# Optimization experiments

Hardware: AMD Instinct MI355X
Metric: run time of the kernel (lower is better)

The kernel has to match this reference:

```python
import jax, jax.numpy as jnp
import numpy as np
import math

B, L, S, H, E, D = 8, 2048, 2048, 8, 64, 64


def setup_inputs() -> dict:
    key = jax.random.key(0)
    kq, kk, kv = jax.random.split(key, 3)
    return {
        "queries": jax.random.normal(kq, (B, L, H, E), dtype=jnp.float32),
        "keys": jax.random.normal(kk, (B, S, H, E), dtype=jnp.float32),
        "values": jax.random.normal(kv, (B, S, H, D), dtype=jnp.float32),
        "attn_mask": jnp.zeros((B, L, S), dtype=bool),
    }


def reference(queries, keys, values, attn_mask):
    b, l, h, e = queries.shape
    s, d = values.shape[1], values.shape[3]
    scale = 1.0 / math.sqrt(e)  # note: 1/sqrt(E), not 1/sqrt(H*E), faithful to source
    q = queries.reshape(b, l, h * e)            # [B, L, HE]
    k = keys.reshape(b, s, h * e)               # [B, S, HE]
    scores = jnp.einsum("ble,bse->bls", q, k)   # full [B, L, S] score matrix
    scores = jnp.where(attn_mask, -jnp.inf, scores)
    A = jax.nn.softmax(scale * scores, axis=-1)  # dropout is identity at inference
    v = values.reshape(b, s, h * d)             # [B, S, HD]
    out = jnp.einsum("bls,bsd->bld", A, v).reshape(b, l, h, d)
    return out
```

## Files before the change

### kernel.cpp

```cpp
#include <hip/hip_runtime.h>
#include <hip/hip_bf16.h>
#include <stdint.h>

typedef __attribute__((ext_vector_type(8))) short  short8;
typedef __attribute__((ext_vector_type(4))) short  short4v;
typedef __attribute__((ext_vector_type(8))) __bf16 bf16x8;
typedef __attribute__((ext_vector_type(4))) float  f32x4;

#define DEVI static __device__ __forceinline__

constexpr int B_  = 8;
constexpr int L_  = 2048;
constexpr int S_  = 2048;
constexpr int DK  = 512;
constexpr int KVB = 32;
constexpr int QB  = 64;
constexpr int NT  = S_ / KVB;
constexpr int TILE_B = KVB * DK * 2;
constexpr float SCL2 = 0.125f * 1.4426950408889634f;

constexpr size_t KT_OFF = 0;
constexpr size_t VT_OFF = (size_t)B_ * NT * TILE_B;
constexpr size_t AM_OFF = VT_OFF * 2;
constexpr size_t WS_NEED = AM_OFF + (size_t)B_ * L_ * 8;

DEVI short f2bf(float f) {
  __hip_bfloat16 h = __float2bfloat16(f);
  return __builtin_bit_cast(short, h);
}

DEVI void gld16(const void* g, void* l) {
  __builtin_amdgcn_global_load_lds(
      (const __attribute__((address_space(1))) unsigned int*)(uintptr_t)g,
      (__attribute__((address_space(3))) unsigned int*)(uint32_t)(uintptr_t)l,
      16, 0, 0);
}


__global__ __launch_bounds__(256)
void prep_k(const float* __restrict__ K, char* __restrict__ Kt) {
  int gid  = blockIdx.x * 256 + threadIdx.x;
  int o    = (gid & 2047) * 16;
  int tile = gid >> 11;
  int row  = o >> 10;
  int colb = (o & 1023) ^ ((row & 7) << 4);
  const float* src = K + ((size_t)tile * KVB + row) * DK + (colb >> 1);
  float4 a = ((const float4*)src)[0];
  float4 c = ((const float4*)src)[1];
  short8 f;
  f[0] = f2bf(a.x); f[1] = f2bf(a.y); f[2] = f2bf(a.z); f[3] = f2bf(a.w);
  f[4] = f2bf(c.x); f[5] = f2bf(c.y); f[6] = f2bf(c.z); f[7] = f2bf(c.w);
  *(short8*)(Kt + (size_t)tile * TILE_B + o) = f;
}

__global__ __launch_bounds__(256)
void prep_v(const float* __restrict__ V, char* __restrict__ Vt) {
  __shared__ short lv[KVB * DK];
  int tile = blockIdx.x;
  int tid  = threadIdx.x;
  const float* src = V + (size_t)tile * KVB * DK;
  #pragma unroll
  for (int i = 0; i < 16; ++i) {
    int fidx = i * 1024 + tid * 4;
    float4 v = *(const float4*)(src + fidx);
    short4v pk = { f2bf(v.x), f2bf(v.y), f2bf(v.z), f2bf(v.w) };
    *(short4v*)((char*)lv + (size_t)fidx * 2) = pk;
  }
  __syncthreads();
  char* dst = Vt + (size_t)tile * TILE_B;
  #pragma unroll
  for (int j = 0; j < 8; ++j) {
    int o     = tid * 16 + j * 4096;
    int pr    = o >> 7;
    int inner = (o & 127) ^ ((pr & 7) << 4);
    int d     = pr * 2 + (inner >> 6);
    int kv0   = (inner & 63) >> 1;
    short8 f;
    #pragma unroll
    for (int k = 0; k < 8; ++k) f[k] = lv[(kv0 + k) * DK + d];
    *(short8*)(dst + o) = f;
  }
}

__global__ __launch_bounds__(256)
void prep_mask(const unsigned char* __restrict__ M,
               unsigned long long* __restrict__ anyM) {
  int row = blockIdx.x * 4 + (threadIdx.x >> 6);
  int l   = threadIdx.x & 63;
  const unsigned int* p = (const unsigned int*)(M + (size_t)row * S_) + l * 8;
  unsigned int acc = 0;
  #pragma unroll
  for (int k = 0; k < 8; ++k) acc |= p[k];
  unsigned long long bal = __ballot(acc != 0);
  if (l == 0) anyM[row] = bal;
}


__global__ __launch_bounds__(256, 1)
void fattn2(const float* __restrict__ Qg, const char* __restrict__ Kt,
            const char* __restrict__ Vt, const unsigned long long* __restrict__ anyM,
            const unsigned char* __restrict__ Mg, float* __restrict__ Og) {
  __shared__ __attribute__((aligned(16))) char kv_lds[2][2 * TILE_B];
  __shared__ __attribute__((aligned(16))) short pbuf[4][16 * KVB];

  const int tid = threadIdx.x;
  const int w   = tid >> 6;
  const int l   = tid & 63;
  const int l15 = l & 15;
  const int l4  = l >> 4;

  const int bidx = blockIdx.x;
  const int swz  = ((bidx & 7) << 5) + (bidx >> 3);
  const int b    = swz >> 5;
  const int qt   = swz & 31;
  const int qloc = qt * QB + w * 16;

  bf16x8 qf[16];
  {
    const float* qp = Qg + ((size_t)(b * L_ + qloc + l15)) * DK + l4 * 8;
    #pragma unroll
    for (int c = 0; c < 16; ++c) {
      float4 a  = *(const float4*)(qp + c * 32);
      float4 bq = *(const float4*)(qp + c * 32 + 4);
      short8 f;
      f[0] = f2bf(a.x);  f[1] = f2bf(a.y);  f[2] = f2bf(a.z);  f[3] = f2bf(a.w);
      f[4] = f2bf(bq.x); f[5] = f2bf(bq.y); f[6] = f2bf(bq.z); f[7] = f2bf(bq.w);
      qf[c] = __builtin_bit_cast(bf16x8, f);
    }
  }
  const unsigned long long mbits = anyM[(size_t)b * L_ + qloc + l15];

  f32x4 acc[32];
  #pragma unroll
  for (int i = 0; i < 32; ++i) acc[i] = f32x4{0.f, 0.f, 0.f, 0.f};
  float mrow[4] = {-__builtin_inff(), -__builtin_inff(), -__builtin_inff(), -__builtin_inff()};
  float lrow[4] = {0.f, 0.f, 0.f, 0.f};

  const char* Ktb = Kt + (size_t)b * NT * TILE_B;
  const char* Vtb = Vt + (size_t)b * NT * TILE_B;
  const unsigned char* Mb = Mg + (size_t)b * L_ * S_;

  const int bKu  = (l15 << 10) + (l4 << 4);
  const int swzK = (l15 & 7) << 4;
  const int bV = (((l15 >> 1) << 7) + ((l15 & 1) << 6) + (l4 << 4)) ^ (((l15 >> 1) & 7) << 4);
  const int bP = l15 * 64 + l4 * 16;

  auto stage = [&](int t, char* buf) {
    const char* ks = Ktb + (size_t)t * TILE_B + w * 1024 + l * 16;
    const char* vs = Vtb + (size_t)t * TILE_B + w * 1024 + l * 16;
    char* kd = buf + w * 1024;
    char* vd = buf + TILE_B + w * 1024;
    #pragma unroll
    for (int r = 0; r < 8; ++r) gld16(ks + r * 4096, kd + r * 4096);
    #pragma unroll
    for (int r = 0; r < 8; ++r) gld16(vs + r * 4096, vd + r * 4096);
  };

  stage(0, kv_lds[0]);
  stage(1, kv_lds[1]);

  for (int t = 0; t < NT; ++t) {
    if (t < NT - 1) asm volatile("s_waitcnt vmcnt(16)" ::: "memory");
    else            asm volatile("s_waitcnt vmcnt(0)"  ::: "memory");
    __builtin_amdgcn_s_barrier();
    asm volatile("" ::: "memory");

    const char* kb = kv_lds[t & 1];
    const char* vb = kv_lds[t & 1] + TILE_B;

    f32x4 s0a = f32x4{0.f, 0.f, 0.f, 0.f};
    f32x4 s0b = f32x4{0.f, 0.f, 0.f, 0.f};
    f32x4 s1a = f32x4{0.f, 0.f, 0.f, 0.f};
    f32x4 s1b = f32x4{0.f, 0.f, 0.f, 0.f};
    #pragma unroll
    for (int c = 0; c < 16; c += 2) {
      int a0 = (bKu + c * 64) ^ swzK;
      int a1 = (bKu + (c + 1) * 64) ^ swzK;
      bf16x8 k0f = *(const bf16x8*)(kb + a0);
      bf16x8 k0g = *(const bf16x8*)(kb + a1);
      bf16x8 k1f = *(const bf16x8*)(kb + a0 + 16384);
      bf16x8 k1g = *(const bf16x8*)(kb + a1 + 16384);
      s0a = __builtin_amdgcn_mfma_f32_16x16x32_bf16(qf[c],     k0f, s0a, 0, 0, 0);
      s1a = __builtin_amdgcn_mfma_f32_16x16x32_bf16(qf[c],     k1f, s1a, 0, 0, 0);
      s0b = __builtin_amdgcn_mfma_f32_16x16x32_bf16(qf[c + 1], k0g, s0b, 0, 0, 0);
      s1b = __builtin_amdgcn_mfma_f32_16x16x32_bf16(qf[c + 1], k1g, s1b, 0, 0, 0);
    }
    float sv0[4], sv1[4];
    #pragma unroll
    for (int r = 0; r < 4; ++r) { sv0[r] = s0a[r] + s0b[r]; sv1[r] = s1a[r] + s1b[r]; }

    if (__any((mbits >> t) & 1ull)) {
      #pragma unroll
      for (int r = 0; r < 4; ++r) {
        const unsigned char* mp = Mb + (size_t)(qloc + l4 * 4 + r) * S_ + (t * KVB + l15);
        if (mp[0])  sv0[r] = -__builtin_inff();
        if (mp[16]) sv1[r] = -__builtin_inff();
      }
    }

    bool need = false;
    float alpha[4];
    #pragma unroll
    for (int r = 0; r < 4; ++r) {
      float tmax = fmaxf(sv0[r], sv1[r]);
      #pragma unroll
      for (int mk = 1; mk < 16; mk <<= 1) tmax = fmaxf(tmax, __shfl_xor(tmax, mk));
      alpha[r] = 1.0f;
      if (tmax > mrow[r]) {
        if ((tmax - mrow[r]) * SCL2 > 8.0f) {
          alpha[r] = exp2f((mrow[r] - tmax) * SCL2);
          mrow[r] = tmax;
          need = true;
        }
      }
    }
    if (__any(need)) {
      #pragma unroll
      for (int dt = 0; dt < 32; ++dt) {
        acc[dt][0] *= alpha[0];
        acc[dt][1] *= alpha[1];
        acc[dt][2] *= alpha[2];
        acc[dt][3] *= alpha[3];
      }
      lrow[0] *= alpha[0]; lrow[1] *= alpha[1];
      lrow[2] *= alpha[2]; lrow[3] *= alpha[3];
    }

    short* pw = pbuf[w];
    #pragma unroll
    for (int r = 0; r < 4; ++r) {
      float p0 = exp2f((sv0[r] - mrow[r]) * SCL2);
      float p1 = exp2f((sv1[r] - mrow[r]) * SCL2);
      lrow[r] += p0 + p1;
      int pr = (l4 * 4 + r) * 32;
      pw[pr + l15]      = f2bf(p0);
      pw[pr + 16 + l15] = f2bf(p1);
    }
    bf16x8 pf = *(const bf16x8*)((const char*)pw + bP);

    #pragma unroll
    for (int dt = 0; dt < 32; ++dt) {
      bf16x8 vf = *(const bf16x8*)(vb + bV + dt * 1024);
      acc[dt] = __builtin_amdgcn_mfma_f32_16x16x32_bf16(pf, vf, acc[dt], 0, 0, 0);
    }

    asm volatile("" ::: "memory");
    __builtin_amdgcn_s_barrier();
    if (t + 2 < NT) stage(t + 2, kv_lds[t & 1]);
  }

  #pragma unroll
  for (int r = 0; r < 4; ++r) {
    float s = lrow[r];
    #pragma unroll
    for (int mk = 1; mk < 16; mk <<= 1) s += __shfl_xor(s, mk);
    lrow[r] = 1.0f / s;
  }
  float* op = Og + ((size_t)(b * L_ + qloc + l4 * 4)) * DK + l15;
  #pragma unroll
  for (int r = 0; r < 4; ++r) {
    #pragma unroll
    for (int dt = 0; dt < 32; ++dt) {
      op[(size_t)r * DK + dt * 16] = acc[dt][r] * lrow[r];
    }
  }
}


__global__ __launch_bounds__(256, 2)
void fattn_kernel(const float* __restrict__ Qg, const float* __restrict__ Kg,
                  const float* __restrict__ Vg, const unsigned char* __restrict__ Mg,
                  float* __restrict__ Og) {
  __shared__ __attribute__((aligned(16))) short kbuf[KVB * DK];
  __shared__ __attribute__((aligned(16))) short vbuf[KVB * DK];
  __shared__ __attribute__((aligned(16))) short pbuf[4][16 * KVB];

  const int tid = threadIdx.x;
  const int w   = tid >> 6;
  const int l   = tid & 63;
  const int l15 = l & 15;
  const int l4  = l >> 4;

  const int b    = blockIdx.y;
  const int qloc = blockIdx.x * QB + w * 16;

  bf16x8 qf[16];
  {
    const float* qp = Qg + ((size_t)(b * L_ + qloc + l15)) * DK + l4 * 8;
    #pragma unroll
    for (int c = 0; c < 16; ++c) {
      float4 a  = *(const float4*)(qp + c * 32);
      float4 bq = *(const float4*)(qp + c * 32 + 4);
      short8 f;
      f[0] = f2bf(a.x);  f[1] = f2bf(a.y);  f[2] = f2bf(a.z);  f[3] = f2bf(a.w);
      f[4] = f2bf(bq.x); f[5] = f2bf(bq.y); f[6] = f2bf(bq.z); f[7] = f2bf(bq.w);
      qf[c] = __builtin_bit_cast(bf16x8, f);
    }
  }

  f32x4 acc[32];
  #pragma unroll
  for (int i = 0; i < 32; ++i) acc[i] = f32x4{0.f, 0.f, 0.f, 0.f};
  float mrow[4] = {-__builtin_inff(), -__builtin_inff(), -__builtin_inff(), -__builtin_inff()};
  float lrow[4] = {0.f, 0.f, 0.f, 0.f};

  const float* Kb = Kg + (size_t)b * S_ * DK;
  const float* Vb = Vg + (size_t)b * S_ * DK;
  const unsigned char* Mb = Mg + (size_t)b * L_ * S_;

  const int bKu  = (l15 << 10) + (l4 << 4);
  const int swzK = (l15 & 7) << 4;
  const int bV = (((l15 >> 1) << 7) + ((l15 & 1) << 6) + (l4 << 4)) ^ (((l15 >> 1) & 7) << 4);
  const int bP = l15 * 64 + l4 * 16;

  for (int t = 0; t < S_ / KVB; ++t) {
    const int k0 = t * KVB;
    {
      const float* src = Kb + (size_t)k0 * DK;
      #pragma unroll
      for (int it = 0; it < 16; ++it) {
        int fidx = it * 1024 + tid * 4;
        float4 v = *(const float4*)(src + fidx);
        int row = fidx >> 9;
        int col = fidx & 511;
        int byt = ((row << 10) + (col << 1)) ^ ((row & 7) << 4);
        short4v pk = { f2bf(v.x), f2bf(v.y), f2bf(v.z), f2bf(v.w) };
        *(short4v*)((char*)kbuf + byt) = pk;
      }
    }
    {
      const float* src = Vb + (size_t)k0 * DK;
      #pragma unroll
      for (int h = 0; h < 4; ++h) {
        int task = h * 256 + tid;
        int dblk = task & 127;
        int kvb  = task >> 7;
        const float* sp = src + (size_t)(kvb * 4) * DK + dblk * 4;
        float4 r0 = *(const float4*)(sp);
        float4 r1 = *(const float4*)(sp + DK);
        float4 r2 = *(const float4*)(sp + 2 * DK);
        float4 r3 = *(const float4*)(sp + 3 * DK);
        #pragma unroll
        for (int i = 0; i < 4; ++i) {
          int d = dblk * 4 + i;
          int byt = (((d >> 1) << 7) + ((d & 1) << 6) + ((kvb * 4) << 1))
                    ^ (((d >> 1) & 7) << 4);
          float e0 = (i == 0) ? r0.x : (i == 1) ? r0.y : (i == 2) ? r0.z : r0.w;
          float e1 = (i == 0) ? r1.x : (i == 1) ? r1.y : (i == 2) ? r1.z : r1.w;
          float e2 = (i == 0) ? r2.x : (i == 1) ? r2.y : (i == 2) ? r2.z : r2.w;
          float e3 = (i == 0) ? r3.x : (i == 1) ? r3.y : (i == 2) ? r3.z : r3.w;
          short4v pk = { f2bf(e0), f2bf(e1), f2bf(e2), f2bf(e3) };
          *(short4v*)((char*)vbuf + byt) = pk;
        }
      }
    }
    __syncthreads();

    f32x4 s0a = f32x4{0.f, 0.f, 0.f, 0.f};
    f32x4 s0b = f32x4{0.f, 0.f, 0.f, 0.f};
    f32x4 s1a = f32x4{0.f, 0.f, 0.f, 0.f};
    f32x4 s1b = f32x4{0.f, 0.f, 0.f, 0.f};
    #pragma unroll
    for (int c = 0; c < 16; c += 2) {
      int a0 = (bKu + c * 64) ^ swzK;
      int a1 = (bKu + (c + 1) * 64) ^ swzK;
      bf16x8 k0f = *(const bf16x8*)((const char*)kbuf + a0);
      bf16x8 k0g = *(const bf16x8*)((const char*)kbuf + a1);
      bf16x8 k1f = *(const bf16x8*)((const char*)kbuf + a0 + 16384);
      bf16x8 k1g = *(const bf16x8*)((const char*)kbuf + a1 + 16384);
      s0a = __builtin_amdgcn_mfma_f32_16x16x32_bf16(qf[c],     k0f, s0a, 0, 0, 0);
      s1a = __builtin_amdgcn_mfma_f32_16x16x32_bf16(qf[c],     k1f, s1a, 0, 0, 0);
      s0b = __builtin_amdgcn_mfma_f32_16x16x32_bf16(qf[c + 1], k0g, s0b, 0, 0, 0);
      s1b = __builtin_amdgcn_mfma_f32_16x16x32_bf16(qf[c + 1], k1g, s1b, 0, 0, 0);
    }
    f32x4 s0, s1;
    #pragma unroll
    for (int r = 0; r < 4; ++r) { s0[r] = s0a[r] + s0b[r]; s1[r] = s1a[r] + s1b[r]; }

    float sv0[4], sv1[4];
    #pragma unroll
    for (int r = 0; r < 4; ++r) {
      const unsigned char* mp = Mb + (size_t)(qloc + l4 * 4 + r) * S_ + (k0 + l15);
      float x0 = s0[r], x1 = s1[r];
      if (mp[0])  x0 = -__builtin_inff();
      if (mp[16]) x1 = -__builtin_inff();
      sv0[r] = x0; sv1[r] = x1;
    }

    bool need = false;
    float alpha[4];
    #pragma unroll
    for (int r = 0; r < 4; ++r) {
      float tmax = fmaxf(sv0[r], sv1[r]);
      #pragma unroll
      for (int mk = 1; mk < 16; mk <<= 1) tmax = fmaxf(tmax, __shfl_xor(tmax, mk));
      alpha[r] = 1.0f;
      if (tmax > mrow[r]) {
        if ((tmax - mrow[r]) * SCL2 > 8.0f) {
          alpha[r] = exp2f((mrow[r] - tmax) * SCL2);
          mrow[r] = tmax;
          need = true;
        }
      }
    }
    if (__any(need)) {
      #pragma unroll
      for (int dt = 0; dt < 32; ++dt) {
        acc[dt][0] *= alpha[0];
        acc[dt][1] *= alpha[1];
        acc[dt][2] *= alpha[2];
        acc[dt][3] *= alpha[3];
      }
      lrow[0] *= alpha[0]; lrow[1] *= alpha[1];
      lrow[2] *= alpha[2]; lrow[3] *= alpha[3];
    }

    short* pw = pbuf[w];
    #pragma unroll
    for (int r = 0; r < 4; ++r) {
      float p0 = exp2f((sv0[r] - mrow[r]) * SCL2);
      float p1 = exp2f((sv1[r] - mrow[r]) * SCL2);
      lrow[r] += p0 + p1;
      int pr = (l4 * 4 + r) * 32;
      pw[pr + l15]      = f2bf(p0);
      pw[pr + 16 + l15] = f2bf(p1);
    }
    bf16x8 pf = *(const bf16x8*)((const char*)pw + bP);

    #pragma unroll
    for (int dt = 0; dt < 32; ++dt) {
      bf16x8 vf = *(const bf16x8*)((const char*)vbuf + (bV + dt * 1024));
      acc[dt] = __builtin_amdgcn_mfma_f32_16x16x32_bf16(pf, vf, acc[dt], 0, 0, 0);
    }
    __syncthreads();
  }

  #pragma unroll
  for (int r = 0; r < 4; ++r) {
    float s = lrow[r];
    #pragma unroll
    for (int mk = 1; mk < 16; mk <<= 1) s += __shfl_xor(s, mk);
    lrow[r] = 1.0f / s;
  }
  float* op = Og + ((size_t)(b * L_ + qloc + l4 * 4)) * DK + l15;
  #pragma unroll
  for (int r = 0; r < 4; ++r) {
    #pragma unroll
    for (int dt = 0; dt < 32; ++dt) {
      op[(size_t)r * DK + dt * 16] = acc[dt][r] * lrow[r];
    }
  }
}


extern "C" void kernel_launch(void* const* d_in, const int* in_sizes, int n_in,
                              void* d_out, int out_size, void* d_ws, size_t ws_size,
                              hipStream_t stream) {
  const float* Q = (const float*)d_in[0];
  const float* K = (const float*)d_in[1];
  const float* V = (const float*)d_in[2];
  const unsigned char* M = (const unsigned char*)d_in[3];
  float* O = (float*)d_out;

  if (ws_size >= WS_NEED) {
    char* ws = (char*)d_ws;
    prep_k   <<<4096, 256, 0, stream>>>(K, ws + KT_OFF);
    prep_v   <<<B_ * NT, 256, 0, stream>>>(V, ws + VT_OFF);
    prep_mask<<<B_ * L_ / 4, 256, 0, stream>>>(M, (unsigned long long*)(ws + AM_OFF));
    fattn2   <<<256, 256, 0, stream>>>(Q, ws + KT_OFF, ws + VT_OFF,
                                       (const unsigned long long*)(ws + AM_OFF), M, O);
  } else {
    dim3 grid(L_ / QB, B_);
    fattn_kernel<<<grid, 256, 0, stream>>>(Q, K, V, M, O);
  }
}
```

Measured before the change: 224.7 us.

## Split KV sequence across two wave groups per block with LDS merge

```diff
diff --git a/kernel.cpp b/kernel.cpp
--- a/kernel.cpp
+++ b/kernel.cpp
@@ -16,6 +16,7 @@
 constexpr int KVB = 32;
 constexpr int QB  = 64;
 constexpr int NT  = S_ / KVB;
+constexpr int NT2 = NT / 2;
 constexpr int TILE_B = KVB * DK * 2;
 constexpr float SCL2 = 0.125f * 1.4426950408889634f;
 
@@ -23,6 +24,14 @@
 constexpr size_t VT_OFF = (size_t)B_ * NT * TILE_B;
 constexpr size_t AM_OFF = VT_OFF * 2;
 constexpr size_t WS_NEED = AM_OFF + (size_t)B_ * L_ * 8;
+
+constexpr int LDS_K0  = 0;
+constexpr int LDS_K1  = 32768;
+constexpr int LDS_V0  = 65536;
+constexpr int LDS_V1  = 98304;
+constexpr int LDS_PB  = 131072;
+constexpr int LDS_MEX = 140288;
+constexpr int LDS_TOT = 141312;
 
 DEVI short f2bf(float f) {
   __hip_bfloat16 h = __float2bfloat16(f);
@@ -96,15 +105,16 @@
 }
 
 
-__global__ __launch_bounds__(256, 1)
-void fattn2(const float* __restrict__ Qg, const char* __restrict__ Kt,
+__global__ __launch_bounds__(512, 2)
+void fattn3(const float* __restrict__ Qg, const char* __restrict__ Kt,
             const char* __restrict__ Vt, const unsigned long long* __restrict__ anyM,
             const unsigned char* __restrict__ Mg, float* __restrict__ Og) {
-  __shared__ __attribute__((aligned(16))) char kv_lds[2][2 * TILE_B];
-  __shared__ __attribute__((aligned(16))) short pbuf[4][16 * KVB];
+  __shared__ __attribute__((aligned(16))) char LDS[LDS_TOT];
 
   const int tid = threadIdx.x;
   const int w   = tid >> 6;
+  const int wl  = w & 3;
+  const int g   = w >> 2;
   const int l   = tid & 63;
   const int l15 = l & 15;
   const int l4  = l >> 4;
@@ -113,7 +123,7 @@
   const int swz  = ((bidx & 7) << 5) + (bidx >> 3);
   const int b    = swz >> 5;
   const int qt   = swz & 31;
-  const int qloc = qt * QB + w * 16;
+  const int qloc = qt * QB + wl * 16;
 
   bf16x8 qf[16];
   {
@@ -140,33 +150,37 @@
   const char* Vtb = Vt + (size_t)b * NT * TILE_B;
   const unsigned char* Mb = Mg + (size_t)b * L_ * S_;
 
+  const char* kb = LDS + (g ? LDS_K1 : LDS_K0);
+  const char* vb = LDS + (g ? LDS_V1 : LDS_V0);
+  short* pw = (short*)(LDS + LDS_PB) + w * (16 * 36);
+
   const int bKu  = (l15 << 10) + (l4 << 4);
   const int swzK = (l15 & 7) << 4;
   const int bV = (((l15 >> 1) << 7) + ((l15 & 1) << 6) + (l4 << 4)) ^ (((l15 >> 1) & 7) << 4);
-  const int bP = l15 * 64 + l4 * 16;
-
-  auto stage = [&](int t, char* buf) {
-    const char* ks = Ktb + (size_t)t * TILE_B + w * 1024 + l * 16;
-    const char* vs = Vtb + (size_t)t * TILE_B + w * 1024 + l * 16;
-    char* kd = buf + w * 1024;
-    char* vd = buf + TILE_B + w * 1024;
-    #pragma unroll
-    for (int r = 0; r < 8; ++r) gld16(ks + r * 4096, kd + r * 4096);
-    #pragma unroll
-    for (int r = 0; r < 8; ++r) gld16(vs + r * 4096, vd + r * 4096);
+  const int bP = l15 * 72 + l4 * 16;
+
+  auto stageK = [&](int t) {
+    const char* ks = Ktb + (size_t)t * TILE_B + wl * 8192 + l * 16;
+    char* kd = (char*)kb + wl * 8192;
+    #pragma unroll
+    for (int r = 0; r < 8; ++r) gld16(ks + r * 1024, kd + r * 1024);
   };
-
-  stage(0, kv_lds[0]);
-  stage(1, kv_lds[1]);
-
-  for (int t = 0; t < NT; ++t) {
-    if (t < NT - 1) asm volatile("s_waitcnt vmcnt(16)" ::: "memory");
-    else            asm volatile("s_waitcnt vmcnt(0)"  ::: "memory");
+  auto stageV = [&](int t) {
+    const char* vs = Vtb + (size_t)t * TILE_B + wl * 8192 + l * 16;
+    char* vd = (char*)vb + wl * 8192;
+    #pragma unroll
+    for (int r = 0; r < 8; ++r) gld16(vs + r * 1024, vd + r * 1024);
+  };
+
+  stageK(g);
+  stageV(g);
+
+  for (int i = 0; i < NT2; ++i) {
+    const int t = 2 * i + g;
+
+    asm volatile("s_waitcnt vmcnt(8)" ::: "memory");
     __builtin_amdgcn_s_barrier();
     asm volatile("" ::: "memory");
-
-    const char* kb = kv_lds[t & 1];
-    const char* vb = kv_lds[t & 1] + TILE_B;
 
     f32x4 s0a = f32x4{0.f, 0.f, 0.f, 0.f};
     f32x4 s0b = f32x4{0.f, 0.f, 0.f, 0.f};
@@ -189,6 +203,10 @@
     #pragma unroll
     for (int r = 0; r < 4; ++r) { sv0[r] = s0a[r] + s0b[r]; sv1[r] = s1a[r] + s1b[r]; }
 
+    asm volatile("" ::: "memory");
+    __builtin_amdgcn_s_barrier();
+    if (i + 1 < NT2) stageK(t + 2);
+
     if (__any((mbits >> t) & 1ull)) {
       #pragma unroll
       for (int r = 0; r < 4; ++r) {
@@ -226,17 +244,21 @@
       lrow[2] *= alpha[2]; lrow[3] *= alpha[3];
     }
 
-    short* pw = pbuf[w];
     #pragma unroll
     for (int r = 0; r < 4; ++r) {
       float p0 = exp2f((sv0[r] - mrow[r]) * SCL2);
       float p1 = exp2f((sv1[r] - mrow[r]) * SCL2);
       lrow[r] += p0 + p1;
-      int pr = (l4 * 4 + r) * 32;
+      int pr = (l4 * 4 + r) * 36;
       pw[pr + l15]      = f2bf(p0);
       pw[pr + 16 + l15] = f2bf(p1);
     }
     bf16x8 pf = *(const bf16x8*)((const char*)pw + bP);
+
+    if (i + 1 < NT2) asm volatile("s_waitcnt vmcnt(8)" ::: "memory");
+    else             asm volatile("s_waitcnt vmcnt(0)" ::: "memory");
+    __builtin_amdgcn_s_barrier();
+    asm volatile("" ::: "memory");
 
     #pragma unroll
     for (int dt = 0; dt < 32; ++dt) {
@@ -246,7 +268,7 @@
 
     asm volatile("" ::: "memory");
     __builtin_amdgcn_s_barrier();
-    if (t + 2 < NT) stage(t + 2, kv_lds[t & 1]);
+    if (i + 1 < NT2) stageV(t + 2);
   }
 
   #pragma unroll
@@ -254,14 +276,56 @@
     float s = lrow[r];
     #pragma unroll
     for (int mk = 1; mk < 16; mk <<= 1) s += __shfl_xor(s, mk);
-    lrow[r] = 1.0f / s;
-  }
+    lrow[r] = s;
+  }
+
+  float* mex = (float*)(LDS + LDS_MEX);
+  if (l15 == 0) {
+    #pragma unroll
+    for (int r = 0; r < 4; ++r) {
+      mex[(w * 16 + l4 * 4 + r) * 2 + 0] = mrow[r];
+      mex[(w * 16 + l4 * 4 + r) * 2 + 1] = lrow[r];
+    }
+  }
+  asm volatile("" ::: "memory");
+  __builtin_amdgcn_s_barrier();
+  asm volatile("" ::: "memory");
+
+  const int pwav = w ^ 4;
+  float asf[4], linv[4];
+  #pragma unroll
+  for (int r = 0; r < 4; ++r) {
+    float mo = mex[(pwav * 16 + l4 * 4 + r) * 2 + 0];
+    float lo = mex[(pwav * 16 + l4 * 4 + r) * 2 + 1];
+    float mst = fmaxf(mrow[r], mo);
+    float a_s = exp2f((mrow[r] - mst) * SCL2);
+    float a_o = exp2f((mo - mst) * SCL2);
+    asf[r]  = a_s;
+    linv[r] = 1.0f / (a_s * lrow[r] + a_o * lo);
+  }
+
+  float* mg = (float*)LDS + (size_t)wl * (16 * 521);
+  const int dbase = g ? 16 : 0;
+  #pragma unroll
+  for (int r = 0; r < 4; ++r) {
+    #pragma unroll
+    for (int dt = 0; dt < 16; ++dt) {
+      mg[(l4 * 4 + r) * 521 + (dbase + dt) * 16 + l15] = asf[r] * acc[dbase + dt][r];
+    }
+  }
+  asm volatile("" ::: "memory");
+  __builtin_amdgcn_s_barrier();
+  asm volatile("" ::: "memory");
+
+  const int sbase = g ? 0 : 16;
   float* op = Og + ((size_t)(b * L_ + qloc + l4 * 4)) * DK + l15;
   #pragma unroll
   for (int r = 0; r < 4; ++r) {
     #pragma unroll
-    for (int dt = 0; dt < 32; ++dt) {
-      op[(size_t)r * DK + dt * 16] = acc[dt][r] * lrow[r];
+    for (int dt = 0; dt < 16; ++dt) {
+      int dd = sbase + dt;
+      float v = (asf[r] * acc[dd][r] + mg[(l4 * 4 + r) * 521 + dd * 16 + l15]) * linv[r];
+      op[(size_t)r * DK + dd * 16] = v;
     }
   }
 }
@@ -415,17 +479,17 @@
       lrow[2] *= alpha[2]; lrow[3] *= alpha[3];
     }
 
-    short* pw = pbuf[w];
+    short* pws = pbuf[w];
     #pragma unroll
     for (int r = 0; r < 4; ++r) {
       float p0 = exp2f((sv0[r] - mrow[r]) * SCL2);
       float p1 = exp2f((sv1[r] - mrow[r]) * SCL2);
       lrow[r] += p0 + p1;
       int pr = (l4 * 4 + r) * 32;
-      pw[pr + l15]      = f2bf(p0);
-      pw[pr + 16 + l15] = f2bf(p1);
-    }
-    bf16x8 pf = *(const bf16x8*)((const char*)pw + bP);
+      pws[pr + l15]      = f2bf(p0);
+      pws[pr + 16 + l15] = f2bf(p1);
+    }
+    bf16x8 pf = *(const bf16x8*)((const char*)pws + bP);
 
     #pragma unroll
     for (int dt = 0; dt < 32; ++dt) {
@@ -467,7 +531,7 @@
     prep_k   <<<4096, 256, 0, stream>>>(K, ws + KT_OFF);
     prep_v   <<<B_ * NT, 256, 0, stream>>>(V, ws + VT_OFF);
     prep_mask<<<B_ * L_ / 4, 256, 0, stream>>>(M, (unsigned long long*)(ws + AM_OFF));
-    fattn2   <<<256, 256, 0, stream>>>(Q, ws + KT_OFF, ws + VT_OFF,
+    fattn3   <<<256, 512, 0, stream>>>(Q, ws + KT_OFF, ws + VT_OFF,
                                        (const unsigned long long*)(ws + AM_OFF), M, O);
   } else {
     dim3 grid(L_ / QB, B_);
```

Result: slower. 331.0 us (+47.3%).

## Split attention work across wave pairs, halving QK depth and PV width per wave

Applied to the files above, without the earlier changes.

```diff
diff --git a/kernel.cpp b/kernel.cpp
--- a/kernel.cpp
+++ b/kernel.cpp
@@ -23,6 +23,12 @@
 constexpr size_t VT_OFF = (size_t)B_ * NT * TILE_B;
 constexpr size_t AM_OFF = VT_OFF * 2;
 constexpr size_t WS_NEED = AM_OFF + (size_t)B_ * L_ * 8;
+
+constexpr int LDS_BUF0 = 0;
+constexpr int LDS_BUF1 = 65536;
+constexpr int LDS_SX   = 131072;
+constexpr int LDS_PB   = 147456;
+constexpr int LDS_TOT  = 152064;
 
 DEVI short f2bf(float f) {
   __hip_bfloat16 h = __float2bfloat16(f);
@@ -97,53 +103,67 @@
 
 
 __global__ __launch_bounds__(256, 1)
-void fattn2(const float* __restrict__ Qg, const char* __restrict__ Kt,
+void fattn4(const float* __restrict__ Qg, const char* __restrict__ Kt,
             const char* __restrict__ Vt, const unsigned long long* __restrict__ anyM,
             const unsigned char* __restrict__ Mg, float* __restrict__ Og) {
-  __shared__ __attribute__((aligned(16))) char kv_lds[2][2 * TILE_B];
-  __shared__ __attribute__((aligned(16))) short pbuf[4][16 * KVB];
-
-  const int tid = threadIdx.x;
-  const int w   = tid >> 6;
-  const int l   = tid & 63;
-  const int l15 = l & 15;
-  const int l4  = l >> 4;
+  __shared__ __attribute__((aligned(16))) char LDS[LDS_TOT];
+
+  const int tid  = threadIdx.x;
+  const int w    = tid >> 6;
+  const int pair = w >> 1;
+  const int half = w & 1;
+  const int l    = tid & 63;
+  const int l15  = l & 15;
+  const int l4   = l >> 4;
 
   const int bidx = blockIdx.x;
   const int swz  = ((bidx & 7) << 5) + (bidx >> 3);
   const int b    = swz >> 5;
   const int qt   = swz & 31;
-  const int qloc = qt * QB + w * 16;
-
-  bf16x8 qf[16];
-  {
-    const float* qp = Qg + ((size_t)(b * L_ + qloc + l15)) * DK + l4 * 8;
-    #pragma unroll
-    for (int c = 0; c < 16; ++c) {
+  const int qrow = qt * QB + pair * 32;
+
+  bf16x8 qf[2][8];
+  #pragma unroll
+  for (int rg = 0; rg < 2; ++rg) {
+    const float* qp = Qg + ((size_t)(b * L_ + qrow + rg * 16 + l15)) * DK
+                      + half * 256 + l4 * 8;
+    #pragma unroll
+    for (int c = 0; c < 8; ++c) {
       float4 a  = *(const float4*)(qp + c * 32);
       float4 bq = *(const float4*)(qp + c * 32 + 4);
       short8 f;
       f[0] = f2bf(a.x);  f[1] = f2bf(a.y);  f[2] = f2bf(a.z);  f[3] = f2bf(a.w);
       f[4] = f2bf(bq.x); f[5] = f2bf(bq.y); f[6] = f2bf(bq.z); f[7] = f2bf(bq.w);
-      qf[c] = __builtin_bit_cast(bf16x8, f);
-    }
-  }
-  const unsigned long long mbits = anyM[(size_t)b * L_ + qloc + l15];
-
-  f32x4 acc[32];
-  #pragma unroll
-  for (int i = 0; i < 32; ++i) acc[i] = f32x4{0.f, 0.f, 0.f, 0.f};
-  float mrow[4] = {-__builtin_inff(), -__builtin_inff(), -__builtin_inff(), -__builtin_inff()};
-  float lrow[4] = {0.f, 0.f, 0.f, 0.f};
+      qf[rg][c] = __builtin_bit_cast(bf16x8, f);
+    }
+  }
+  const unsigned long long mb0 = anyM[(size_t)b * L_ + qrow + l15];
+  const unsigned long long mb1 = anyM[(size_t)b * L_ + qrow + 16 + l15];
+  const unsigned long long mbAny = mb0 | mb1;
+
+  f32x4 acc[2][16];
+  #pragma unroll
+  for (int rg = 0; rg < 2; ++rg)
+    #pragma unroll
+    for (int dt = 0; dt < 16; ++dt) acc[rg][dt] = f32x4{0.f, 0.f, 0.f, 0.f};
+  float mrow[2][4], lrow[2][4];
+  #pragma unroll
+  for (int rg = 0; rg < 2; ++rg)
+    #pragma unroll
+    for (int r = 0; r < 4; ++r) { mrow[rg][r] = -__builtin_inff(); lrow[rg][r] = 0.f; }
 
   const char* Ktb = Kt + (size_t)b * NT * TILE_B;
   const char* Vtb = Vt + (size_t)b * NT * TILE_B;
   const unsigned char* Mb = Mg + (size_t)b * L_ * S_;
 
-  const int bKu  = (l15 << 10) + (l4 << 4);
+  char* sx_own = LDS + LDS_SX + (pair * 2 + half) * 4096 + l * 16;
+  char* sx_par = LDS + LDS_SX + (pair * 2 + (half ^ 1)) * 4096 + l * 16;
+  short* pw = (short*)(LDS + LDS_PB) + pair * (32 * 36);
+
   const int swzK = (l15 & 7) << 4;
-  const int bV = (((l15 >> 1) << 7) + ((l15 & 1) << 6) + (l4 << 4)) ^ (((l15 >> 1) & 7) << 4);
-  const int bP = l15 * 64 + l4 * 16;
+  const int bKu  = (l15 << 10) + (half * 512) + (l4 << 4);
+  const int bV   = ((((l15 >> 1) << 7) + ((l15 & 1) << 6) + (l4 << 4))
+                    ^ (((l15 >> 1) & 7) << 4)) + half * 16384;
 
   auto stage = [&](int t, char* buf) {
     const char* ks = Ktb + (size_t)t * TILE_B + w * 1024 + l * 16;
@@ -156,8 +176,8 @@
     for (int r = 0; r < 8; ++r) gld16(vs + r * 4096, vd + r * 4096);
   };
 
-  stage(0, kv_lds[0]);
-  stage(1, kv_lds[1]);
+  stage(0, LDS + LDS_BUF0);
+  stage(1, LDS + LDS_BUF1);
 
   for (int t = 0; t < NT; ++t) {
     if (t < NT - 1) asm volatile("s_waitcnt vmcnt(16)" ::: "memory");
@@ -165,103 +185,137 @@
     __builtin_amdgcn_s_barrier();
     asm volatile("" ::: "memory");
 
-    const char* kb = kv_lds[t & 1];
-    const char* vb = kv_lds[t & 1] + TILE_B;
-
-    f32x4 s0a = f32x4{0.f, 0.f, 0.f, 0.f};
-    f32x4 s0b = f32x4{0.f, 0.f, 0.f, 0.f};
-    f32x4 s1a = f32x4{0.f, 0.f, 0.f, 0.f};
-    f32x4 s1b = f32x4{0.f, 0.f, 0.f, 0.f};
-    #pragma unroll
-    for (int c = 0; c < 16; c += 2) {
+    const char* kb = LDS + ((t & 1) ? LDS_BUF1 : LDS_BUF0);
+    const char* vb = kb + TILE_B;
+
+    f32x4 s[2][2];
+    #pragma unroll
+    for (int rg = 0; rg < 2; ++rg)
+      #pragma unroll
+      for (int kvg = 0; kvg < 2; ++kvg) s[rg][kvg] = f32x4{0.f, 0.f, 0.f, 0.f};
+    __builtin_amdgcn_s_setprio(1);
+    #pragma unroll
+    for (int c = 0; c < 8; ++c) {
       int a0 = (bKu + c * 64) ^ swzK;
-      int a1 = (bKu + (c + 1) * 64) ^ swzK;
       bf16x8 k0f = *(const bf16x8*)(kb + a0);
-      bf16x8 k0g = *(const bf16x8*)(kb + a1);
       bf16x8 k1f = *(const bf16x8*)(kb + a0 + 16384);
-      bf16x8 k1g = *(const bf16x8*)(kb + a1 + 16384);
-      s0a = __builtin_amdgcn_mfma_f32_16x16x32_bf16(qf[c],     k0f, s0a, 0, 0, 0);
-      s1a = __builtin_amdgcn_mfma_f32_16x16x32_bf16(qf[c],     k1f, s1a, 0, 0, 0);
-      s0b = __builtin_amdgcn_mfma_f32_16x16x32_bf16(qf[c + 1], k0g, s0b, 0, 0, 0);
-      s1b = __builtin_amdgcn_mfma_f32_16x16x32_bf16(qf[c + 1], k1g, s1b, 0, 0, 0);
-    }
-    float sv0[4], sv1[4];
-    #pragma unroll
-    for (int r = 0; r < 4; ++r) { sv0[r] = s0a[r] + s0b[r]; sv1[r] = s1a[r] + s1b[r]; }
-
-    if (__any((mbits >> t) & 1ull)) {
-      #pragma unroll
-      for (int r = 0; r < 4; ++r) {
-        const unsigned char* mp = Mb + (size_t)(qloc + l4 * 4 + r) * S_ + (t * KVB + l15);
-        if (mp[0])  sv0[r] = -__builtin_inff();
-        if (mp[16]) sv1[r] = -__builtin_inff();
-      }
-    }
-
-    bool need = false;
-    float alpha[4];
-    #pragma unroll
-    for (int r = 0; r < 4; ++r) {
-      float tmax = fmaxf(sv0[r], sv1[r]);
-      #pragma unroll
-      for (int mk = 1; mk < 16; mk <<= 1) tmax = fmaxf(tmax, __shfl_xor(tmax, mk));
-      alpha[r] = 1.0f;
-      if (tmax > mrow[r]) {
-        if ((tmax - mrow[r]) * SCL2 > 8.0f) {
-          alpha[r] = exp2f((mrow[r] - tmax) * SCL2);
-          mrow[r] = tmax;
-          need = true;
-        }
-      }
-    }
-    if (__any(need)) {
-      #pragma unroll
-      for (int dt = 0; dt < 32; ++dt) {
-        acc[dt][0] *= alpha[0];
-        acc[dt][1] *= alpha[1];
-        acc[dt][2] *= alpha[2];
-        acc[dt][3] *= alpha[3];
-      }
-      lrow[0] *= alpha[0]; lrow[1] *= alpha[1];
-      lrow[2] *= alpha[2]; lrow[3] *= alpha[3];
-    }
-
-    short* pw = pbuf[w];
-    #pragma unroll
-    for (int r = 0; r < 4; ++r) {
-      float p0 = exp2f((sv0[r] - mrow[r]) * SCL2);
-      float p1 = exp2f((sv1[r] - mrow[r]) * SCL2);
-      lrow[r] += p0 + p1;
-      int pr = (l4 * 4 + r) * 32;
-      pw[pr + l15]      = f2bf(p0);
-      pw[pr + 16 + l15] = f2bf(p1);
-    }
-    bf16x8 pf = *(const bf16x8*)((const char*)pw + bP);
-
-    #pragma unroll
-    for (int dt = 0; dt < 32; ++dt) {
-      bf16x8 vf = *(const bf16x8*)(vb + bV + dt * 1024);
-      acc[dt] = __builtin_amdgcn_mfma_f32_16x16x32_bf16(pf, vf, acc[dt], 0, 0, 0);
-    }
-
+      s[0][0] = __builtin_amdgcn_mfma_f32_16x16x32_bf16(qf[0][c], k0f, s[0][0], 0, 0, 0);
+      s[0][1] = __builtin_amdgcn_mfma_f32_16x16x32_bf16(qf[0][c], k1f, s[0][1], 0, 0, 0);
+      s[1][0] = __builtin_amdgcn_mfma_f32_16x16x32_bf16(qf[1][c], k0f, s[1][0], 0, 0, 0);
+      s[1][1] = __builtin_amdgcn_mfma_f32_16x16x32_bf16(qf[1][c], k1f, s[1][1], 0, 0, 0);
+    }
+    __builtin_amdgcn_s_setprio(0);
+
+    #pragma unroll
+    for (int rg = 0; rg < 2; ++rg)
+      #pragma unroll
+      for (int kvg = 0; kvg < 2; ++kvg)
+        *(f32x4*)(sx_own + (rg * 2 + kvg) * 1024) = s[rg][kvg];
     asm volatile("" ::: "memory");
     __builtin_amdgcn_s_barrier();
-    if (t + 2 < NT) stage(t + 2, kv_lds[t & 1]);
-  }
-
-  #pragma unroll
-  for (int r = 0; r < 4; ++r) {
-    float s = lrow[r];
-    #pragma unroll
-    for (int mk = 1; mk < 16; mk <<= 1) s += __shfl_xor(s, mk);
-    lrow[r] = 1.0f / s;
-  }
-  float* op = Og + ((size_t)(b * L_ + qloc + l4 * 4)) * DK + l15;
-  #pragma unroll
-  for (int r = 0; r < 4; ++r) {
-    #pragma unroll
-    for (int dt = 0; dt < 32; ++dt) {
-      op[(size_t)r * DK + dt * 16] = acc[dt][r] * lrow[r];
+    asm volatile("" ::: "memory");
+    #pragma unroll
+    for (int rg = 0; rg < 2; ++rg)
+      #pragma unroll
+      for (int kvg = 0; kvg < 2; ++kvg) {
+        f32x4 o = *(const f32x4*)(sx_par + (rg * 2 + kvg) * 1024);
+        s[rg][kvg][0] += o[0]; s[rg][kvg][1] += o[1];
+        s[rg][kvg][2] += o[2]; s[rg][kvg][3] += o[3];
+      }
+
+    if (__any((mbAny >> t) & 1ull)) {
+      #pragma unroll
+      for (int rg = 0; rg < 2; ++rg)
+        #pragma unroll
+        for (int r = 0; r < 4; ++r) {
+          const unsigned char* mp = Mb
+            + (size_t)(qrow + rg * 16 + l4 * 4 + r) * S_ + (t * KVB + l15);
+          if (mp[0])  s[rg][0][r] = -__builtin_inff();
+          if (mp[16]) s[rg][1][r] = -__builtin_inff();
+        }
+    }
+
+    bool need = false;
+    float alpha[2][4];
+    #pragma unroll
+    for (int rg = 0; rg < 2; ++rg)
+      #pragma unroll
+      for (int r = 0; r < 4; ++r) {
+        float tmax = fmaxf(s[rg][0][r], s[rg][1][r]);
+        #pragma unroll
+        for (int mk = 1; mk < 16; mk <<= 1) tmax = fmaxf(tmax, __shfl_xor(tmax, mk));
+        alpha[rg][r] = 1.0f;
+        if (tmax > mrow[rg][r]) {
+          if ((tmax - mrow[rg][r]) * SCL2 > 8.0f) {
+            alpha[rg][r] = exp2f((mrow[rg][r] - tmax) * SCL2);
+            mrow[rg][r] = tmax;
+            need = true;
+          }
+        }
+      }
+    if (__any(need)) {
+      #pragma unroll
+      for (int rg = 0; rg < 2; ++rg)
+        #pragma unroll
+        for (int dt = 0; dt < 16; ++dt) {
+          acc[rg][dt][0] *= alpha[rg][0];
+          acc[rg][dt][1] *= alpha[rg][1];
+          acc[rg][dt][2] *= alpha[rg][2];
+          acc[rg][dt][3] *= alpha[rg][3];
+        }
+      #pragma unroll
+      for (int rg = 0; rg < 2; ++rg)
+        #pragma unroll
+        for (int r = 0; r < 4; ++r) lrow[rg][r] *= alpha[rg][r];
+    }
+
+    #pragma unroll
+    for (int rg = 0; rg < 2; ++rg)
+      #pragma unroll
+      for (int r = 0; r < 4; ++r) {
+        float p0 = exp2f((s[rg][0][r] - mrow[rg][r]) * SCL2);
+        float p1 = exp2f((s[rg][1][r] - mrow[rg][r]) * SCL2);
+        lrow[rg][r] += p0 + p1;
+        int qr = (rg * 16 + l4 * 4 + r) * 36;
+        pw[qr + l15]      = f2bf(p0);
+        pw[qr + 16 + l15] = f2bf(p1);
+      }
+    bf16x8 pf0 = *(const bf16x8*)((const char*)pw + l15 * 72 + l4 * 16);
+    bf16x8 pf1 = *(const bf16x8*)((const char*)pw + (16 + l15) * 72 + l4 * 16);
+
+    __builtin_amdgcn_s_setprio(1);
+    #pragma unroll
+    for (int dt = 0; dt < 16; ++dt) {
+      bf16x8 vf = *(const bf16x8*)(vb + bV + dt * 1024);
+      acc[0][dt] = __builtin_amdgcn_mfma_f32_16x16x32_bf16(pf0, vf, acc[0][dt], 0, 0, 0);
+      acc[1][dt] = __builtin_amdgcn_mfma_f32_16x16x32_bf16(pf1, vf, acc[1][dt], 0, 0, 0);
+    }
+    __builtin_amdgcn_s_setprio(0);
+
+    asm volatile("" ::: "memory");
+    __builtin_amdgcn_s_barrier();
+    if (t + 2 < NT) stage(t + 2, LDS + ((t & 1) ? LDS_BUF1 : LDS_BUF0));
+  }
+
+  #pragma unroll
+  for (int rg = 0; rg < 2; ++rg)
+    #pragma unroll
+    for (int r = 0; r < 4; ++r) {
+      float sum = lrow[rg][r];
+      #pragma unroll
+      for (int mk = 1; mk < 16; mk <<= 1) sum += __shfl_xor(sum, mk);
+      lrow[rg][r] = 1.0f / sum;
+    }
+  #pragma unroll
+  for (int rg = 0; rg < 2; ++rg) {
+    float* op = Og + ((size_t)(b * L_ + qrow + rg * 16 + l4 * 4)) * DK
+                + half * 256 + l15;
+    #pragma unroll
+    for (int r = 0; r < 4; ++r) {
+      #pragma unroll
+      for (int dt = 0; dt < 16; ++dt) {
+        op[(size_t)r * DK + dt * 16] = acc[rg][dt][r] * lrow[rg][r];
+      }
     }
   }
 }
@@ -415,17 +469,17 @@
       lrow[2] *= alpha[2]; lrow[3] *= alpha[3];
     }
 
-    short* pw = pbuf[w];
+    short* pws = pbuf[w];
     #pragma unroll
     for (int r = 0; r < 4; ++r) {
       float p0 = exp2f((sv0[r] - mrow[r]) * SCL2);
       float p1 = exp2f((sv1[r] - mrow[r]) * SCL2);
       lrow[r] += p0 + p1;
       int pr = (l4 * 4 + r) * 32;
-      pw[pr + l15]      = f2bf(p0);
-      pw[pr + 16 + l15] = f2bf(p1);
-    }
-    bf16x8 pf = *(const bf16x8*)((const char*)pw + bP);
+      pws[pr + l15]      = f2bf(p0);
+      pws[pr + 16 + l15] = f2bf(p1);
+    }
+    bf16x8 pf = *(const bf16x8*)((const char*)pws + bP);
 
     #pragma unroll
     for (int dt = 0; dt < 32; ++dt) {
@@ -467,7 +521,7 @@
     prep_k   <<<4096, 256, 0, stream>>>(K, ws + KT_OFF);
     prep_v   <<<B_ * NT, 256, 0, stream>>>(V, ws + VT_OFF);
     prep_mask<<<B_ * L_ / 4, 256, 0, stream>>>(M, (unsigned long long*)(ws + AM_OFF));
-    fattn2   <<<256, 256, 0, stream>>>(Q, ws + KT_OFF, ws + VT_OFF,
+    fattn4   <<<256, 256, 0, stream>>>(Q, ws + KT_OFF, ws + VT_OFF,
                                        (const unsigned long long*)(ws + AM_OFF), M, O);
   } else {
     dim3 grid(L_ / QB, B_);
```

Measured after the change: 301.5 us. +34.2%, slower.

## Software-pipeline QK^T for next tile alongside softmax and PV of current tile

Applied to the files above, without the earlier changes.

```diff
diff --git a/kernel.cpp b/kernel.cpp
--- a/kernel.cpp
+++ b/kernel.cpp
@@ -23,6 +23,13 @@
 constexpr size_t VT_OFF = (size_t)B_ * NT * TILE_B;
 constexpr size_t AM_OFF = VT_OFF * 2;
 constexpr size_t WS_NEED = AM_OFF + (size_t)B_ * L_ * 8;
+
+constexpr int LDS_K0 = 0;
+constexpr int LDS_K1 = 32768;
+constexpr int LDS_V0 = 65536;
+constexpr int LDS_V1 = 98304;
+constexpr int LDS_PB = 131072;
+constexpr int LDS_TOT = 135168;
 
 DEVI short f2bf(float f) {
   __hip_bfloat16 h = __float2bfloat16(f);
@@ -97,11 +104,10 @@
 
 
 __global__ __launch_bounds__(256, 1)
-void fattn2(const float* __restrict__ Qg, const char* __restrict__ Kt,
+void fattn5(const float* __restrict__ Qg, const char* __restrict__ Kt,
             const char* __restrict__ Vt, const unsigned long long* __restrict__ anyM,
             const unsigned char* __restrict__ Mg, float* __restrict__ Og) {
-  __shared__ __attribute__((aligned(16))) char kv_lds[2][2 * TILE_B];
-  __shared__ __attribute__((aligned(16))) short pbuf[4][16 * KVB];
+  __shared__ __attribute__((aligned(16))) char LDS[LDS_TOT];
 
   const int tid = threadIdx.x;
   const int w   = tid >> 6;
@@ -140,54 +146,78 @@
   const char* Vtb = Vt + (size_t)b * NT * TILE_B;
   const unsigned char* Mb = Mg + (size_t)b * L_ * S_;
 
+  short* pw = (short*)(LDS + LDS_PB) + w * (16 * 32);
+
   const int bKu  = (l15 << 10) + (l4 << 4);
   const int swzK = (l15 & 7) << 4;
   const int bV = (((l15 >> 1) << 7) + ((l15 & 1) << 6) + (l4 << 4)) ^ (((l15 >> 1) & 7) << 4);
   const int bP = l15 * 64 + l4 * 16;
 
-  auto stage = [&](int t, char* buf) {
-    const char* ks = Ktb + (size_t)t * TILE_B + w * 1024 + l * 16;
-    const char* vs = Vtb + (size_t)t * TILE_B + w * 1024 + l * 16;
-    char* kd = buf + w * 1024;
-    char* vd = buf + TILE_B + w * 1024;
-    #pragma unroll
-    for (int r = 0; r < 8; ++r) gld16(ks + r * 4096, kd + r * 4096);
-    #pragma unroll
-    for (int r = 0; r < 8; ++r) gld16(vs + r * 4096, vd + r * 4096);
+  auto stageK = [&](int t, char* buf) {
+    const char* ks = Ktb + (size_t)t * TILE_B + w * 8192 + l * 16;
+    char* kd = buf + w * 8192;
+    #pragma unroll
+    for (int r = 0; r < 8; ++r) gld16(ks + r * 1024, kd + r * 1024);
   };
-
-  stage(0, kv_lds[0]);
-  stage(1, kv_lds[1]);
+  auto stageV = [&](int t, char* buf) {
+    const char* vs = Vtb + (size_t)t * TILE_B + w * 8192 + l * 16;
+    char* vd = buf + w * 8192;
+    #pragma unroll
+    for (int r = 0; r < 8; ++r) gld16(vs + r * 1024, vd + r * 1024);
+  };
+
+  stageK(0, LDS + LDS_K0);
+  stageV(0, LDS + LDS_V0);
+  stageK(1, LDS + LDS_K1);
+  stageV(1, LDS + LDS_V1);
+
+  asm volatile("s_waitcnt vmcnt(24)" ::: "memory");
+  __builtin_amdgcn_s_barrier();
+  asm volatile("" ::: "memory");
+
+  f32x4 sv0q = f32x4{0.f, 0.f, 0.f, 0.f};
+  f32x4 sv1q = f32x4{0.f, 0.f, 0.f, 0.f};
+  {
+    const char* k0b = LDS + LDS_K0;
+    #pragma unroll
+    for (int c = 0; c < 16; ++c) {
+      int a0 = (bKu + c * 64) ^ swzK;
+      bf16x8 k0f = *(const bf16x8*)(k0b + a0);
+      bf16x8 k1f = *(const bf16x8*)(k0b + a0 + 16384);
+      sv0q = __builtin_amdgcn_mfma_f32_16x16x32_bf16(qf[c], k0f, sv0q, 0, 0, 0);
+      sv1q = __builtin_amdgcn_mfma_f32_16x16x32_bf16(qf[c], k1f, sv1q, 0, 0, 0);
+    }
+  }
+  asm volatile("" ::: "memory");
+  __builtin_amdgcn_s_barrier();
+  stageK(2, LDS + LDS_K0);
 
   for (int t = 0; t < NT; ++t) {
-    if (t < NT - 1) asm volatile("s_waitcnt vmcnt(16)" ::: "memory");
-    else            asm volatile("s_waitcnt vmcnt(0)"  ::: "memory");
+    if (t <= NT - 3)      asm volatile("s_waitcnt vmcnt(16)" ::: "memory");
+    else if (t == NT - 2) asm volatile("s_waitcnt vmcnt(8)"  ::: "memory");
+    else                  asm volatile("s_waitcnt vmcnt(0)"  ::: "memory");
     __builtin_amdgcn_s_barrier();
     asm volatile("" ::: "memory");
 
-    const char* kb = kv_lds[t & 1];
-    const char* vb = kv_lds[t & 1] + TILE_B;
-
-    f32x4 s0a = f32x4{0.f, 0.f, 0.f, 0.f};
-    f32x4 s0b = f32x4{0.f, 0.f, 0.f, 0.f};
-    f32x4 s1a = f32x4{0.f, 0.f, 0.f, 0.f};
-    f32x4 s1b = f32x4{0.f, 0.f, 0.f, 0.f};
-    #pragma unroll
-    for (int c = 0; c < 16; c += 2) {
-      int a0 = (bKu + c * 64) ^ swzK;
-      int a1 = (bKu + (c + 1) * 64) ^ swzK;
-      bf16x8 k0f = *(const bf16x8*)(kb + a0);
-      bf16x8 k0g = *(const bf16x8*)(kb + a1);
-      bf16x8 k1f = *(const bf16x8*)(kb + a0 + 16384);
-      bf16x8 k1g = *(const bf16x8*)(kb + a1 + 16384);
-      s0a = __builtin_amdgcn_mfma_f32_16x16x32_bf16(qf[c],     k0f, s0a, 0, 0, 0);
-      s1a = __builtin_amdgcn_mfma_f32_16x16x32_bf16(qf[c],     k1f, s1a, 0, 0, 0);
-      s0b = __builtin_amdgcn_mfma_f32_16x16x32_bf16(qf[c + 1], k0g, s0b, 0, 0, 0);
-      s1b = __builtin_amdgcn_mfma_f32_16x16x32_bf16(qf[c + 1], k1g, s1b, 0, 0, 0);
-    }
+    const char* vb = LDS + ((t & 1) ? LDS_V1 : LDS_V0);
+
+    f32x4 n0 = f32x4{0.f, 0.f, 0.f, 0.f};
+    f32x4 n1 = f32x4{0.f, 0.f, 0.f, 0.f};
+    if (t < NT - 1) {
+      const char* kn = LDS + (((t + 1) & 1) ? LDS_K1 : LDS_K0);
+      #pragma unroll
+      for (int c = 0; c < 16; ++c) {
+        int a0 = (bKu + c * 64) ^ swzK;
+        bf16x8 k0f = *(const bf16x8*)(kn + a0);
+        bf16x8 k1f = *(const bf16x8*)(kn + a0 + 16384);
+        n0 = __builtin_amdgcn_mfma_f32_16x16x32_bf16(qf[c], k0f, n0, 0, 0, 0);
+        n1 = __builtin_amdgcn_mfma_f32_16x16x32_bf16(qf[c], k1f, n1, 0, 0, 0);
+      }
+    }
+
     float sv0[4], sv1[4];
     #pragma unroll
-    for (int r = 0; r < 4; ++r) { sv0[r] = s0a[r] + s0b[r]; sv1[r] = s1a[r] + s1b[r]; }
+    for (int r = 0; r < 4; ++r) { sv0[r] = sv0q[r]; sv1[r] = sv1q[r]; }
 
     if (__any((mbits >> t) & 1ull)) {
       #pragma unroll
@@ -226,7 +256,6 @@
       lrow[2] *= alpha[2]; lrow[3] *= alpha[3];
     }
 
-    short* pw = pbuf[w];
     #pragma unroll
     for (int r = 0; r < 4; ++r) {
       float p0 = exp2f((sv0[r] - mrow[r]) * SCL2);
@@ -244,9 +273,13 @@
       acc[dt] = __builtin_amdgcn_mfma_f32_16x16x32_bf16(pf, vf, acc[dt], 0, 0, 0);
     }
 
+    sv0q = n0;
+    sv1q = n1;
+
     asm volatile("" ::: "memory");
     __builtin_amdgcn_s_barrier();
-    if (t + 2 < NT) stage(t + 2, kv_lds[t & 1]);
+    if (t + 3 < NT) stageK(t + 3, LDS + (((t + 1) & 1) ? LDS_K1 : LDS_K0));
+    if (t + 2 < NT) stageV(t + 2, LDS + ((t & 1) ? LDS_V1 : LDS_V0));
   }
 
   #pragma unroll
@@ -415,17 +448,17 @@
       lrow[2] *= alpha[2]; lrow[3] *= alpha[3];
     }
 
-    short* pw = pbuf[w];
+    short* pws = pbuf[w];
     #pragma unroll
     for (int r = 0; r < 4; ++r) {
       float p0 = exp2f((sv0[r] - mrow[r]) * SCL2);
       float p1 = exp2f((sv1[r] - mrow[r]) * SCL2);
       lrow[r] += p0 + p1;
       int pr = (l4 * 4 + r) * 32;
-      pw[pr + l15]      = f2bf(p0);
-      pw[pr + 16 + l15] = f2bf(p1);
-    }
-    bf16x8 pf = *(const bf16x8*)((const char*)pw + bP);
+      pws[pr + l15]      = f2bf(p0);
+      pws[pr + 16 + l15] = f2bf(p1);
+    }
+    bf16x8 pf = *(const bf16x8*)((const char*)pws + bP);
 
     #pragma unroll
     for (int dt = 0; dt < 32; ++dt) {
@@ -467,7 +500,7 @@
     prep_k   <<<4096, 256, 0, stream>>>(K, ws + KT_OFF);
     prep_v   <<<B_ * NT, 256, 0, stream>>>(V, ws + VT_OFF);
     prep_mask<<<B_ * L_ / 4, 256, 0, stream>>>(M, (unsigned long long*)(ws + AM_OFF));
-    fattn2   <<<256, 256, 0, stream>>>(Q, ws + KT_OFF, ws + VT_OFF,
+    fattn5   <<<256, 256, 0, stream>>>(Q, ws + KT_OFF, ws + VT_OFF,
                                        (const unsigned long long*)(ws + AM_OFF), M, O);
   } else {
     dim3 grid(L_ / QB, B_);
```

Result: slower. 233.2 us (median of 2 runs) (+3.8%).
